# Kernel optimization log

Measured on AMD Instinct MI355X. Metric: run time of the kernel, lower is better.

The kernel has to match this reference:

```python
import jax, jax.numpy as jnp
import numpy as np
from jax import lax

TOP_NUMBER = 5
MOMENTUM = 0.1
EPS = 1e-12  # F.normalize eps


def _normalize(x):
    # F.normalize(x, dim=1): x / max(||x||_2, eps)
    n = jnp.sqrt(jnp.sum(x * x, axis=1, keepdims=True))
    return x / jnp.maximum(n, EPS)


def _cos_distance(a, b):
    # 0.5 * (1 - cos_sim); a:[B,D], b:[N,D] -> [B,N]
    a = _normalize(a)
    b = _normalize(b)
    return 0.5 * (1.0 - jnp.matmul(a, b.T))


def setup_inputs() -> dict:
    key = jax.random.key(0)
    ks = jax.random.split(key, 6)
    B, D, C, N = 64, 256, 345, 200000
    return {
        "target_feature": jax.random.normal(ks[0], (B, D), dtype=jnp.float32),
        "fc1": jax.random.normal(ks[1], (B, C), dtype=jnp.float32),
        "fc2": jax.random.normal(ks[2], (B, C), dtype=jnp.float32),
        "index_target": jnp.arange(B, dtype=jnp.int64 if jax.config.jax_enable_x64 else jnp.int32),
        "target_featurememory": jax.random.normal(ks[3], (N, D), dtype=jnp.float32),
        "target_softmaxFc1memory": jax.random.uniform(ks[4], (N, C), dtype=jnp.float32),
        "target_softmaxFc2memory": jax.random.uniform(ks[5], (N, C), dtype=jnp.float32),
    }


def reference(target_feature, fc1, fc2, index_target,
              target_featurememory, target_softmaxFc1memory, target_softmaxFc2memory):
    k = TOP_NUMBER
    m = MOMENTUM

    # predict(): softmax first
    fc1 = jax.nn.softmax(fc1, axis=1)
    fc2 = jax.nn.softmax(fc2, axis=1)

    # update(): momentum scatter-update of the memory banks (uses .data, i.e. detached)
    feat_mem = target_featurememory.at[index_target].set(
        (1.0 - m) * target_featurememory[index_target] + m * target_feature)
    fc1_mem = target_softmaxFc1memory.at[index_target].set(
        (1.0 - m) * target_softmaxFc1memory[index_target] + m * fc1)
    fc2_mem = target_softmaxFc2memory.at[index_target].set(
        (1.0 - m) * target_softmaxFc2memory[index_target] + m * fc2)

    # feature_smiliarity: nearest (smallest cos-distance) features, drop self (first)
    d_feat = _cos_distance(target_feature, feat_mem)          # [B, N]
    _, idx = lax.top_k(-d_feat, k + 1)                         # smallest distances
    idx = idx[:, 1:].reshape(-1)                               # [B*k]
    fc1_gather = fc1_mem[idx]                                  # [B*k, C]
    fc2_gather = fc2_mem[idx]
    loss_softmax = jnp.mean(jnp.abs(fc1_gather - fc2_gather))  # Discrepancy (L1)

    # softmax_smiliarity: topk of size k, then drop first -> k-1 neighbors
    d1 = _cos_distance(fc1, fc1_mem)                           # [B, N]
    _, i1 = lax.top_k(-d1, k)
    i1 = i1[:, 1:].reshape(-1)                                 # [B*(k-1)]
    feat1 = feat_mem[i1]                                       # [B*(k-1), D]

    d2 = _cos_distance(fc2, fc2_mem)
    _, i2 = lax.top_k(-d2, k)
    i2 = i2[:, 1:].reshape(-1)
    feat2 = feat_mem[i2]

    # FeatureDistance: 0.5 * (1 - <norm(a), norm(b)>) per row, then mean
    fd = 0.5 * (1.0 - jnp.sum(_normalize(feat1) * _normalize(feat2), axis=1))
    loss_feature = jnp.mean(fd)

    return (loss_softmax, loss_feature)
```

## Files before the change

### kernel.cpp

```cpp
#include <hip/hip_runtime.h>
#include <hip/hip_bf16.h>
#include <float.h>
#include <math.h>

#define NQ    64
#define DF    256
#define CC    345
#define KSF   8
#define KSC   11
#define NBM   768
#define FRESH (1 << 30)
#define EPSN  1e-12f

typedef __attribute__((ext_vector_type(8))) short short8;
typedef __attribute__((ext_vector_type(4))) float f32x4;

__device__ __forceinline__ void gld16(const void* g, void* l) {
  __builtin_amdgcn_global_load_lds(
      static_cast<const uint32_t*>(g), static_cast<uint32_t*>(l), 16, 0, 0);
}
__device__ __forceinline__ void gld4(const void* g, void* l) {
  __builtin_amdgcn_global_load_lds(
      static_cast<const uint32_t*>(g), static_cast<uint32_t*>(l), 4, 0, 0);
}

__device__ __forceinline__ float blockReduceSum(float v, float* sbuf) {
  __syncthreads();
  #pragma unroll
  for (int o = 32; o > 0; o >>= 1) v += __shfl_down(v, o);
  int w = threadIdx.x >> 6;
  if ((threadIdx.x & 63) == 0) sbuf[w] = v;
  __syncthreads();
  if (threadIdx.x == 0) {
    float s = 0.f;
    int nw = blockDim.x >> 6;
    for (int i = 0; i < nw; ++i) s += sbuf[i];
    sbuf[0] = s;
  }
  __syncthreads();
  return sbuf[0];
}

__device__ __forceinline__ float blockReduceMax(float v, float* sbuf) {
  __syncthreads();
  #pragma unroll
  for (int o = 32; o > 0; o >>= 1) v = fmaxf(v, __shfl_down(v, o));
  int w = threadIdx.x >> 6;
  if ((threadIdx.x & 63) == 0) sbuf[w] = v;
  __syncthreads();
  if (threadIdx.x == 0) {
    float s = -FLT_MAX;
    int nw = blockDim.x >> 6;
    for (int i = 0; i < nw; ++i) s = fmaxf(s, sbuf[i]);
    sbuf[0] = s;
  }
  __syncthreads();
  return sbuf[0];
}

template<int T>
__device__ __forceinline__ void topk_insert(float v, int id, float (&lv)[T], int (&li)[T]) {
  if (!((v > lv[T-1]) || (v == lv[T-1] && id < li[T-1]))) return;
  #pragma unroll
  for (int p = T-1; p > 0; --p) {
    bool up = (v > lv[p-1]) || (v == lv[p-1] && id < li[p-1]);
    if (up) { lv[p] = lv[p-1]; li[p] = li[p-1]; }
    else    { lv[p] = v; li[p] = id; return; }
  }
  lv[0] = v; li[0] = id;
}

template<int T>
__device__ __forceinline__ void merge4(const float* sv, const int* si, int t,
                                       float* dv, int* di) {
  float fv[T]; int fi[T];
  #pragma unroll
  for (int i = 0; i < T; ++i) { fv[i] = -FLT_MAX; fi[i] = 0x7fffffff; }
  for (int s = 0; s < 4; ++s)
    #pragma unroll
    for (int i = 0; i < T; ++i)
      topk_insert<T>(sv[(t*4+s)*T+i], si[(t*4+s)*T+i], fv, fi);
  #pragma unroll
  for (int i = 0; i < T; ++i) { dv[t*T+i] = fv[i]; di[t*T+i] = fi[i]; }
}

__global__ void fill_rowmap(int* rowmap, int n) {
  int i = blockIdx.x * blockDim.x + threadIdx.x;
  if (i < n) rowmap[i] = -1;
}

__global__ __launch_bounds__(384) void prep_kernel(
    const float* __restrict__ tf, const float* __restrict__ fc1,
    const float* __restrict__ fc2, const int* __restrict__ idx,
    const float* __restrict__ featm, const float* __restrict__ fc1m,
    const float* __restrict__ fc2m,
    short* __restrict__ Qp_feat, short* __restrict__ Qp_fc1, short* __restrict__ Qp_fc2,
    float* __restrict__ featU, float* __restrict__ fc1U, float* __restrict__ fc2U,
    int* __restrict__ rowmap)
{
  __shared__ float sbuf[8];
  const int b = blockIdx.x, t = threadIdx.x;
  const int trow = idx[b];
  const int qt = b >> 4, qr = b & 15;

  {
    float x = (t < DF) ? tf[b*DF + t] : 0.f;
    float ss = blockReduceSum(x*x, sbuf);
    float inv = 1.f / fmaxf(sqrtf(ss), EPSN);
    if (t < DF) {
      featU[b*DF + t] = 0.9f * featm[(size_t)trow*DF + t] + 0.1f * x;
      int ks = t >> 5, lg = (t >> 3) & 3, j = t & 7;
      int lane = qr + lg*16;
      union { __hip_bfloat16 h; short s; } cv;
      cv.h = __float2bfloat16(x * inv);
      Qp_feat[((qt*KSF + ks)*64 + lane)*8 + j] = cv.s;
    }
  }
  {
    float y = (t < CC) ? fc1[b*CC + t] : -FLT_MAX;
    float mx = blockReduceMax(y, sbuf);
    float e = (t < CC) ? expf(y - mx) : 0.f;
    float se = blockReduceSum(e, sbuf);
    float s = e / se;
    float s2 = blockReduceSum(s*s, sbuf);
    float inv2 = 1.f / fmaxf(sqrtf(s2), EPSN);
    if (t < CC) fc1U[b*CC + t] = 0.9f * fc1m[(size_t)trow*CC + t] + 0.1f * s;
    if (t < KSC*32) {
      int ks = t >> 5, lg = (t >> 3) & 3, j = t & 7;
      int lane = qr + lg*16;
      union { __hip_bfloat16 h; short s; } cv;
      cv.h = __float2bfloat16((t < CC) ? s * inv2 : 0.f);
      Qp_fc1[((qt*KSC + ks)*64 + lane)*8 + j] = cv.s;
    }
  }
  {
    float y = (t < CC) ? fc2[b*CC + t] : -FLT_MAX;
    float mx = blockReduceMax(y, sbuf);
    float e = (t < CC) ? expf(y - mx) : 0.f;
    float se = blockReduceSum(e, sbuf);
    float s = e / se;
    float s2 = blockReduceSum(s*s, sbuf);
    float inv2 = 1.f / fmaxf(sqrtf(s2), EPSN);
    if (t < CC) fc2U[b*CC + t] = 0.9f * fc2m[(size_t)trow*CC + t] + 0.1f * s;
    if (t < KSC*32) {
      int ks = t >> 5, lg = (t >> 3) & 3, j = t & 7;
      int lane = qr + lg*16;
      union { __hip_bfloat16 h; short s; } cv;
      cv.h = __float2bfloat16((t < CC) ? s * inv2 : 0.f);
      Qp_fc2[((qt*KSC + ks)*64 + lane)*8 + j] = cv.s;
    }
  }
  if (t == 0) rowmap[trow] = b;
}

template<int D, int KS, int T>
__global__ __launch_bounds__(256, 3) void dist_topk5(
    const float* __restrict__ bank, const float* __restrict__ ubank,
    const int* __restrict__ uids, const short8* __restrict__ Qp,
    float* __restrict__ cand_v, int* __restrict__ cand_i,
    int nmain, int ntq, int ntr)
{
  constexpr bool FEAT = (D == 256);
  constexpr int GROW = D * 4;
  constexpr int SROW = FEAT ? 1024 : 1392;
  constexpr int BUFB = 16 * SROW;

  __shared__ __align__(16) char smem[2*BUFB + 128 + 2*64*17*4];
  char*  k344 = smem + 2*BUFB;
  float* sims = (float*)(smem + 2*BUFB + 128);
  float* mv   = (float*)smem;
  int*   mi   = (int*)(smem + 256*T*4);

  const int t = threadIdx.x, l = t & 63, w = t >> 6;
  const int lc = l & 15, lg = l >> 4;
  const bool corr = ((int)blockIdx.x >= nmain);
  const float* srcb = corr ? ubank : bank;

  int tile0, nt;
  if (corr) { tile0 = blockIdx.x - nmain; nt = 1; }
  else {
    int b = blockIdx.x;
    tile0 = b*ntq + (b < ntr ? b : ntr);
    nt = ntq + (b < ntr ? 1 : 0);
  }

  short8 afr[KS];
  #pragma unroll
  for (int ks = 0; ks < KS; ++ks) afr[ks] = Qp[(w*KS + ks)*64 + l];

  auto STAGE = [&](int tile, int pn) {
    const char* tb = (const char*)srcb + (size_t)tile * (size_t)(16*GROW);
    char* bb = smem + pn*BUFB;
    #pragma unroll
    for (int r2 = 0; r2 < 4; ++r2) {
      int row = w*4 + r2;
      if (FEAT) {
        gld16(tb + row*1024 + ((l ^ (row & 7)) * 16), bb + row*1024);
      } else {
        gld16(tb + row*1380 + l*16, bb + row*1392);
        if (l < 22) gld16(tb + row*1380 + 1024 + l*16, bb + row*1392 + 1024);
      }
    }
    if (!FEAT && w == 0 && l < 16)
      gld4(tb + l*1380 + 1376, k344 + pn*64);
  };

  STAGE(tile0, 0);
  __syncthreads();

  float lv[T]; int li[T];
  #pragma unroll
  for (int i = 0; i < T; ++i) { lv[i] = -FLT_MAX; li[i] = 0x7fffffff; }

  for (int it = 0; it < nt; ++it) {
    const int pn = it & 1;
    if (it + 1 < nt) STAGE(tile0 + it + 1, pn ^ 1);

    const char* bb = smem + pn*BUFB;
    f32x4 acc = (f32x4){0.f, 0.f, 0.f, 0.f};
    float sq = 0.f;

    #pragma unroll
    for (int ks = 0; ks < KS; ++ks) {
      float v[8];
      if (!FEAT && ks == KS-1 && lg == 3) {
        v[0] = *(const float*)(k344 + pn*64 + lc*4);
        #pragma unroll
        for (int j = 1; j < 8; ++j) v[j] = 0.f;
      } else if (FEAT) {
        int g0 = ks*8 + lg*2;
        float4 a = *(const float4*)(bb + lc*1024 + ((g0 ^ (lc & 7)) * 16));
        float4 c = *(const float4*)(bb + lc*1024 + (((g0 + 1) ^ (lc & 7)) * 16));
        v[0]=a.x; v[1]=a.y; v[2]=a.z; v[3]=a.w;
        v[4]=c.x; v[5]=c.y; v[6]=c.z; v[7]=c.w;
      } else {
        const char* p = bb + lc*1392 + ks*128 + lg*32;
        float4 a = *(const float4*)p;
        float4 c = *(const float4*)(p + 16);
        v[0]=a.x; v[1]=a.y; v[2]=a.z; v[3]=a.w;
        v[4]=c.x; v[5]=c.y; v[6]=c.z; v[7]=c.w;
      }
      #pragma unroll
      for (int j = 0; j < 8; ++j) sq += v[j]*v[j];
      union { short8 s8; __hip_bfloat162 h2[4]; } fb;
      #pragma unroll
      for (int j = 0; j < 4; ++j)
        fb.h2[j] = __float22bfloat162_rn(make_float2(v[2*j], v[2*j+1]));
      acc = __builtin_amdgcn_mfma_f32_16x16x32_bf16(afr[ks], fb.s8, acc, 0, 0, 0);
    }

    float s = sq;
    s += __shfl_xor(s, 16);
    s += __shfl_xor(s, 32);
    float ri = 1.f / fmaxf(sqrtf(s), EPSN);

    float* sp = sims + pn*64*17;
    #pragma unroll
    for (int rg = 0; rg < 4; ++rg)
      sp[(w*16 + lg*4 + rg)*17 + lc] = acc[rg] * ri;
    __syncthreads();

    {
      int q = t & 63, sub = t >> 6;
      const float* s2 = sims + pn*64*17 + q*17 + sub*4;
      #pragma unroll
      for (int j = 0; j < 4; ++j) {
        int r = sub*4 + j;
        int id = corr ? (uids[tile0*16 + r] | FRESH) : ((tile0 + it)*16 + r);
        topk_insert<T>(s2[j], id, lv, li);
      }
    }
  }
  __syncthreads();

  #pragma unroll
  for (int i = 0; i < T; ++i) { mv[t*T + i] = lv[i]; mi[t*T + i] = li[i]; }
  __syncthreads();
  if (t < 64) {
    float fv[T]; int fi[T];
    #pragma unroll
    for (int i = 0; i < T; ++i) { fv[i] = -FLT_MAX; fi[i] = 0x7fffffff; }
    for (int s = 0; s < 4; ++s) {
      int srcidx = t + 64*s;
      #pragma unroll
      for (int i = 0; i < T; ++i)
        topk_insert<T>(mv[srcidx*T + i], mi[srcidx*T + i], fv, fi);
    }
    size_t base = ((size_t)blockIdx.x*64 + t)*T;
    #pragma unroll
    for (int i = 0; i < T; ++i) { cand_v[base + i] = fv[i]; cand_i[base + i] = fi[i]; }
  }
}

template<int T>
__global__ __launch_bounds__(256) void merge_stage1(
    const float* __restrict__ cv, const int* __restrict__ ci,
    const int* __restrict__ rowmap, int nslots,
    float* __restrict__ midv, int* __restrict__ midi)
{
  __shared__ float sv[256*T]; __shared__ int si[256*T];
  __shared__ float sv2[64*T]; __shared__ int si2[64*T];
  const int q = blockIdx.x >> 3, s = blockIdx.x & 7, t = threadIdx.x;
  const int len = (nslots + 7) >> 3;
  const int lo = s*len, hi = min(nslots, lo + len);
  float lv[T]; int li[T];
  #pragma unroll
  for (int i = 0; i < T; ++i) { lv[i] = -FLT_MAX; li[i] = 0x7fffffff; }
  for (int c = lo + t; c < hi; c += 256) {
    size_t base = ((size_t)c*64 + q)*T;
    #pragma unroll
    for (int i = 0; i < T; ++i) {
      int id = ci[base + i];
      if ((id & FRESH) || rowmap[id] < 0)
        topk_insert<T>(cv[base + i], id, lv, li);
    }
  }
  #pragma unroll
  for (int i = 0; i < T; ++i) { sv[t*T+i] = lv[i]; si[t*T+i] = li[i]; }
  __syncthreads();
  if (t < 64) merge4<T>(sv, si, t, sv2, si2);
  __syncthreads();
  if (t < 16) merge4<T>(sv2, si2, t, sv, si);
  __syncthreads();
  if (t < 4)  merge4<T>(sv, si, t, sv2, si2);
  __syncthreads();
  if (t == 0) {
    float fv[T]; int fi[T];
    #pragma unroll
    for (int i = 0; i < T; ++i) { fv[i] = -FLT_MAX; fi[i] = 0x7fffffff; }
    for (int c = 0; c < 4*T; ++c) topk_insert<T>(sv2[c], si2[c], fv, fi);
    #pragma unroll
    for (int i = 0; i < T; ++i) {
      midv[blockIdx.x*T + i] = fv[i];
      midi[blockIdx.x*T + i] = fi[i];
    }
  }
}

template<int T>
__global__ __launch_bounds__(64) void merge_stage2(
    const float* __restrict__ midv, const int* __restrict__ midi,
    int* __restrict__ topout)
{
  __shared__ float sv[8*T]; __shared__ int si[8*T];
  const int q = blockIdx.x, t = threadIdx.x;
  if (t < 8*T) { sv[t] = midv[q*8*T + t]; si[t] = midi[q*8*T + t]; }
  __syncthreads();
  if (t == 0) {
    float fv[T]; int fi[T];
    #pragma unroll
    for (int i = 0; i < T; ++i) { fv[i] = -FLT_MAX; fi[i] = 0x7fffffff; }
    for (int c = 0; c < 8*T; ++c) topk_insert<T>(sv[c], si[c], fv, fi);
    #pragma unroll
    for (int i = 0; i < T; ++i) topout[q*6 + i] = fi[i] & ~FRESH;
  }
}

__global__ __launch_bounds__(384) void loss_softmax_kernel(
    const int* __restrict__ topfeat, const int* __restrict__ rowmap,
    const float* __restrict__ fc1m, const float* __restrict__ fc1U,
    const float* __restrict__ fc2m, const float* __restrict__ fc2U,
    float* __restrict__ out)
{
  __shared__ float sbuf[8];
  int p = blockIdx.x;
  int q = p / 5, j = p % 5 + 1;
  int row = topfeat[q*6 + j];
  int u = rowmap[row];
  const float* r1 = (u >= 0) ? (fc1U + (size_t)u * CC) : (fc1m + (size_t)row * CC);
  const float* r2 = (u >= 0) ? (fc2U + (size_t)u * CC) : (fc2m + (size_t)row * CC);
  int t = threadIdx.x;
  float v = (t < CC) ? fabsf(r1[t] - r2[t]) : 0.f;
  float s = blockReduceSum(v, sbuf);
  if (t == 0) atomicAdd(out, s * (1.f / (320.f * 345.f)));
}

__global__ __launch_bounds__(256) void loss_feature_kernel(
    const int* __restrict__ topfc1, const int* __restrict__ topfc2,
    const int* __restrict__ rowmap, const float* __restrict__ featm,
    const float* __restrict__ featU, float* __restrict__ out)
{
  __shared__ float sbuf[8];
  int p = blockIdx.x;
  int q = p / 4, j = p % 4 + 1;
  int ra = topfc1[q*6 + j], rb = topfc2[q*6 + j];
  int ua = rowmap[ra], ub = rowmap[rb];
  const float* A  = (ua >= 0) ? (featU + (size_t)ua * DF) : (featm + (size_t)ra * DF);
  const float* Bp = (ub >= 0) ? (featU + (size_t)ub * DF) : (featm + (size_t)rb * DF);
  int t = threadIdx.x;
  float a = A[t], b = Bp[t];
  float saa = blockReduceSum(a*a, sbuf);
  float sbb = blockReduceSum(b*b, sbuf);
  float sab = blockReduceSum(a*b, sbuf);
  if (t == 0) {
    float fd = 0.5f * (1.f - sab / (fmaxf(sqrtf(saa), EPSN) * fmaxf(sqrtf(sbb), EPSN)));
    atomicAdd(out + 1, fd * (1.f / 256.f));
  }
}

extern "C" void kernel_launch(void* const* d_in, const int* in_sizes, int n_in,
                              void* d_out, int out_size, void* d_ws, size_t ws_size,
                              hipStream_t stream)
{
  const float* tf    = (const float*)d_in[0];
  const float* fc1   = (const float*)d_in[1];
  const float* fc2   = (const float*)d_in[2];
  const int*   idx   = (const int*)d_in[3];
  const float* featm = (const float*)d_in[4];
  const float* fc1m  = (const float*)d_in[5];
  const float* fc2m  = (const float*)d_in[6];
  float* out = (float*)d_out;

  const int N     = in_sizes[4] / DF;
  const int TILES = N / 16;
  const int NTQ   = TILES / NBM;
  const int NTR   = TILES - NTQ * NBM;
  const int NSLOT = NBM + 4;

  char* w = (char*)d_ws;
  auto alloc = [&](size_t bytes) {
    char* p = w;
    w += (bytes + 255) & ~(size_t)255;
    return (void*)p;
  };
  short* Qp_feat = (short*)alloc((size_t)4 * KSF * 64 * 8 * 2);
  short* Qp_fc1  = (short*)alloc((size_t)4 * KSC * 64 * 8 * 2);
  short* Qp_fc2  = (short*)alloc((size_t)4 * KSC * 64 * 8 * 2);
  float* featU   = (float*)alloc((size_t)NQ * DF * 4);
  float* fc1U    = (float*)alloc((size_t)NQ * CC * 4);
  float* fc2U    = (float*)alloc((size_t)NQ * CC * 4);
  int*   rowmap  = (int*)alloc((size_t)N * 4);
  int*   topfeat = (int*)alloc(NQ * 6 * 4);
  int*   topfc1  = (int*)alloc(NQ * 6 * 4);
  int*   topfc2  = (int*)alloc(NQ * 6 * 4);
  float* cand_v  = (float*)alloc((size_t)NSLOT * 64 * 6 * 4);
  int*   cand_i  = (int*)alloc((size_t)NSLOT * 64 * 6 * 4);
  float* midv    = (float*)alloc((size_t)NQ * 8 * 6 * 4);
  int*   midi    = (int*)alloc((size_t)NQ * 8 * 6 * 4);

  hipMemsetAsync(d_out, 0, 2 * sizeof(float), stream);
  fill_rowmap<<<(N + 255) / 256, 256, 0, stream>>>(rowmap, N);
  prep_kernel<<<NQ, 384, 0, stream>>>(tf, fc1, fc2, idx, featm, fc1m, fc2m,
      Qp_feat, Qp_fc1, Qp_fc2, featU, fc1U, fc2U, rowmap);

  dist_topk5<DF, KSF, 6><<<NSLOT, 256, 0, stream>>>(
      featm, featU, idx, (const short8*)Qp_feat, cand_v, cand_i, NBM, NTQ, NTR);
  merge_stage1<6><<<NQ*8, 256, 0, stream>>>(cand_v, cand_i, rowmap, NSLOT, midv, midi);
  merge_stage2<6><<<NQ, 64, 0, stream>>>(midv, midi, topfeat);

  dist_topk5<CC, KSC, 5><<<NSLOT, 256, 0, stream>>>(
      fc1m, fc1U, idx, (const short8*)Qp_fc1, cand_v, cand_i, NBM, NTQ, NTR);
  merge_stage1<5><<<NQ*8, 256, 0, stream>>>(cand_v, cand_i, rowmap, NSLOT, midv, midi);
  merge_stage2<5><<<NQ, 64, 0, stream>>>(midv, midi, topfc1);

  dist_topk5<CC, KSC, 5><<<NSLOT, 256, 0, stream>>>(
      fc2m, fc2U, idx, (const short8*)Qp_fc2, cand_v, cand_i, NBM, NTQ, NTR);
  merge_stage1<5><<<NQ*8, 256, 0, stream>>>(cand_v, cand_i, rowmap, NSLOT, midv, midi);
  merge_stage2<5><<<NQ, 64, 0, stream>>>(midv, midi, topfc2);

  loss_softmax_kernel<<<320, 384, 0, stream>>>(topfeat, rowmap, fc1m, fc1U, fc2m, fc2U, out);
  loss_feature_kernel<<<256, 256, 0, stream>>>(topfc1, topfc2, rowmap, featm, featU, out);
}
```

Baseline: 678.2 us.

## Prefetch two tiles ahead with explicit vmcnt waits and raw barriers

Restructures the double-buffered tile loop in the distance/top-k kernel. Two tiles are now staged up front, and each iteration waits on partial vmcnt counts so that the next tile's global-to-LDS loads stay in flight during compute. The next-next tile is issued into the freed buffer right after the sims barrier. It also replaces hipMemsetAsync with a tiny zeroing kernel. The hand-counted waitcnt values depend on exactly how many loads each wave issues, so a miscount could cause reads of stale LDS data.

After: 678.1 us. About the same (-0.0%).

```diff
diff --git a/kernel.cpp b/kernel.cpp
--- a/kernel.cpp
+++ b/kernel.cpp
@@ -22,6 +22,36 @@
 __device__ __forceinline__ void gld4(const void* g, void* l) {
   __builtin_amdgcn_global_load_lds(
       static_cast<const uint32_t*>(g), static_cast<uint32_t*>(l), 4, 0, 0);
+}
+
+__device__ __forceinline__ void wait_vm0() {
+  asm volatile("s_waitcnt vmcnt(0)" ::: "memory");
+  __builtin_amdgcn_sched_barrier(0);
+}
+__device__ __forceinline__ void wait_vm4() {
+  asm volatile("s_waitcnt vmcnt(4)" ::: "memory");
+  __builtin_amdgcn_sched_barrier(0);
+}
+__device__ __forceinline__ void wait_vm8() {
+  asm volatile("s_waitcnt vmcnt(8)" ::: "memory");
+  __builtin_amdgcn_sched_barrier(0);
+}
+__device__ __forceinline__ void wait_vm9() {
+  asm volatile("s_waitcnt vmcnt(9)" ::: "memory");
+  __builtin_amdgcn_sched_barrier(0);
+}
+__device__ __forceinline__ void wait_lgkm0() {
+  asm volatile("s_waitcnt lgkmcnt(0)" ::: "memory");
+  __builtin_amdgcn_sched_barrier(0);
+}
+__device__ __forceinline__ void raw_barrier() {
+  __builtin_amdgcn_sched_barrier(0);
+  __builtin_amdgcn_s_barrier();
+  __builtin_amdgcn_sched_barrier(0);
+}
+
+__global__ void zero_out(float* out) {
+  if (threadIdx.x < 2) out[threadIdx.x] = 0.f;
 }
 
 __device__ __forceinline__ float blockReduceSum(float v, float* sbuf) {
@@ -154,7 +184,7 @@
 }
 
 template<int D, int KS, int T>
-__global__ __launch_bounds__(256, 3) void dist_topk5(
+__global__ __launch_bounds__(256, 3) void dist_topk6(
     const float* __restrict__ bank, const float* __restrict__ ubank,
     const int* __restrict__ uids, const short8* __restrict__ Qp,
     float* __restrict__ cand_v, int* __restrict__ cand_i,
@@ -206,7 +236,7 @@
   };
 
   STAGE(tile0, 0);
-  __syncthreads();
+  if (nt > 1) STAGE(tile0 + 1, 1);
 
   float lv[T]; int li[T];
   #pragma unroll
@@ -214,7 +244,15 @@
 
   for (int it = 0; it < nt; ++it) {
     const int pn = it & 1;
-    if (it + 1 < nt) STAGE(tile0 + it + 1, pn ^ 1);
+
+    if (it + 1 < nt) {
+      if (FEAT) wait_vm4();
+      else if (w == 0) wait_vm9();
+      else wait_vm8();
+    } else {
+      wait_vm0();
+    }
+    raw_barrier();
 
     const char* bb = smem + pn*BUFB;
     f32x4 acc = (f32x4){0.f, 0.f, 0.f, 0.f};
@@ -258,7 +296,11 @@
     #pragma unroll
     for (int rg = 0; rg < 4; ++rg)
       sp[(w*16 + lg*4 + rg)*17 + lc] = acc[rg] * ri;
-    __syncthreads();
+
+    wait_lgkm0();
+    raw_barrier();
+
+    if (it + 2 < nt) STAGE(tile0 + it + 2, pn);
 
     {
       int q = t & 63, sub = t >> 6;
@@ -438,22 +480,22 @@
   float* midv    = (float*)alloc((size_t)NQ * 8 * 6 * 4);
   int*   midi    = (int*)alloc((size_t)NQ * 8 * 6 * 4);
 
-  hipMemsetAsync(d_out, 0, 2 * sizeof(float), stream);
+  zero_out<<<1, 64, 0, stream>>>(out);
   fill_rowmap<<<(N + 255) / 256, 256, 0, stream>>>(rowmap, N);
   prep_kernel<<<NQ, 384, 0, stream>>>(tf, fc1, fc2, idx, featm, fc1m, fc2m,
       Qp_feat, Qp_fc1, Qp_fc2, featU, fc1U, fc2U, rowmap);
 
-  dist_topk5<DF, KSF, 6><<<NSLOT, 256, 0, stream>>>(
+  dist_topk6<DF, KSF, 6><<<NSLOT, 256, 0, stream>>>(
       featm, featU, idx, (const short8*)Qp_feat, cand_v, cand_i, NBM, NTQ, NTR);
   merge_stage1<6><<<NQ*8, 256, 0, stream>>>(cand_v, cand_i, rowmap, NSLOT, midv, midi);
   merge_stage2<6><<<NQ, 64, 0, stream>>>(midv, midi, topfeat);
 
-  dist_topk5<CC, KSC, 5><<<NSLOT, 256, 0, stream>>>(
+  dist_topk6<CC, KSC, 5><<<NSLOT, 256, 0, stream>>>(
       fc1m, fc1U, idx, (const short8*)Qp_fc1, cand_v, cand_i, NBM, NTQ, NTR);
   merge_stage1<5><<<NQ*8, 256, 0, stream>>>(cand_v, cand_i, rowmap, NSLOT, midv, midi);
   merge_stage2<5><<<NQ, 64, 0, stream>>>(midv, midi, topfc1);
 
-  dist_topk5<CC, KSC, 5><<<NSLOT, 256, 0, stream>>>(
+  dist_topk6<CC, KSC, 5><<<NSLOT, 256, 0, stream>>>(
       fc2m, fc2U, idx, (const short8*)Qp_fc2, cand_v, cand_i, NBM, NTQ, NTR);
   merge_stage1<5><<<NQ*8, 256, 0, stream>>>(cand_v, cand_i, rowmap, NSLOT, midv, midi);
   merge_stage2<5><<<NQ, 64, 0, stream>>>(midv, midi, topfc2);
```

## Restructure distance-topk to per-wave tiles with direct global loads

Applied to the files above, without the earlier changes.

Replaces the block-cooperative LDS-staged, double-buffered distance kernel with a per-wave design. Each wave loads its 16-row tile straight from global memory, computes all 64 query columns with four MFMA accumulators, and keeps its own top-k with no block-level syncs or in-block merge. Each wave writes its own candidate slot, which greatly increases the number of candidates merge_stage1 has to process. The aim is to remove __syncthreads and LDS staging overhead and raise occupancy, at the cost of uncoalesced per-lane row loads, query fragments re-read from global memory for every tile, and a heavier merge step.

Measured after the change: 1.129 ms. 1.67x slower.

```diff
diff --git a/kernel.cpp b/kernel.cpp
--- a/kernel.cpp
+++ b/kernel.cpp
@@ -8,20 +8,18 @@
 #define CC    345
 #define KSF   8
 #define KSC   11
-#define NBM   768
+#define BLK   512
+#define NBLK  768
+#define NWAVES (NBLK * (BLK/64))
 #define FRESH (1 << 30)
 #define EPSN  1e-12f
 
 typedef __attribute__((ext_vector_type(8))) short short8;
 typedef __attribute__((ext_vector_type(4))) float f32x4;
-
-__device__ __forceinline__ void gld16(const void* g, void* l) {
-  __builtin_amdgcn_global_load_lds(
-      static_cast<const uint32_t*>(g), static_cast<uint32_t*>(l), 16, 0, 0);
-}
-__device__ __forceinline__ void gld4(const void* g, void* l) {
-  __builtin_amdgcn_global_load_lds(
-      static_cast<const uint32_t*>(g), static_cast<uint32_t*>(l), 4, 0, 0);
+typedef __attribute__((ext_vector_type(4), aligned(4))) float f32x4u;
+
+__global__ void zero_out(float* out) {
+  if (threadIdx.x < 2) out[threadIdx.x] = 0.f;
 }
 
 __device__ __forceinline__ float blockReduceSum(float v, float* sbuf) {
@@ -154,91 +152,45 @@
 }
 
 template<int D, int KS, int T>
-__global__ __launch_bounds__(256, 3) void dist_topk5(
+__global__ __launch_bounds__(BLK, 4) void dist_topk7(
     const float* __restrict__ bank, const float* __restrict__ ubank,
     const int* __restrict__ uids, const short8* __restrict__ Qp,
-    float* __restrict__ cand_v, int* __restrict__ cand_i,
-    int nmain, int ntq, int ntr)
-{
-  constexpr bool FEAT = (D == 256);
-  constexpr int GROW = D * 4;
-  constexpr int SROW = FEAT ? 1024 : 1392;
-  constexpr int BUFB = 16 * SROW;
-
-  __shared__ __align__(16) char smem[2*BUFB + 128 + 2*64*17*4];
-  char*  k344 = smem + 2*BUFB;
-  float* sims = (float*)(smem + 2*BUFB + 128);
-  float* mv   = (float*)smem;
-  int*   mi   = (int*)(smem + 256*T*4);
-
-  const int t = threadIdx.x, l = t & 63, w = t >> 6;
+    float* __restrict__ cand_v, int* __restrict__ cand_i, int ntm)
+{
+  __shared__ __align__(16) float scr[BLK/64][16*68];
+  const int t = threadIdx.x, l = t & 63;
   const int lc = l & 15, lg = l >> 4;
-  const bool corr = ((int)blockIdx.x >= nmain);
-  const float* srcb = corr ? ubank : bank;
-
-  int tile0, nt;
-  if (corr) { tile0 = blockIdx.x - nmain; nt = 1; }
-  else {
-    int b = blockIdx.x;
-    tile0 = b*ntq + (b < ntr ? b : ntr);
-    nt = ntq + (b < ntr ? 1 : 0);
-  }
-
-  short8 afr[KS];
-  #pragma unroll
-  for (int ks = 0; ks < KS; ++ks) afr[ks] = Qp[(w*KS + ks)*64 + l];
-
-  auto STAGE = [&](int tile, int pn) {
-    const char* tb = (const char*)srcb + (size_t)tile * (size_t)(16*GROW);
-    char* bb = smem + pn*BUFB;
-    #pragma unroll
-    for (int r2 = 0; r2 < 4; ++r2) {
-      int row = w*4 + r2;
-      if (FEAT) {
-        gld16(tb + row*1024 + ((l ^ (row & 7)) * 16), bb + row*1024);
-      } else {
-        gld16(tb + row*1380 + l*16, bb + row*1392);
-        if (l < 22) gld16(tb + row*1380 + 1024 + l*16, bb + row*1392 + 1024);
-      }
-    }
-    if (!FEAT && w == 0 && l < 16)
-      gld4(tb + l*1380 + 1376, k344 + pn*64);
-  };
-
-  STAGE(tile0, 0);
-  __syncthreads();
+  const int wloc = t >> 6;
+  const int wid = blockIdx.x * (BLK/64) + wloc;
+  const int TT = ntm + 4;
+  float* myscr = scr[wloc];
 
   float lv[T]; int li[T];
   #pragma unroll
   for (int i = 0; i < T; ++i) { lv[i] = -FLT_MAX; li[i] = 0x7fffffff; }
 
-  for (int it = 0; it < nt; ++it) {
-    const int pn = it & 1;
-    if (it + 1 < nt) STAGE(tile0 + it + 1, pn ^ 1);
-
-    const char* bb = smem + pn*BUFB;
-    f32x4 acc = (f32x4){0.f, 0.f, 0.f, 0.f};
+  for (int tile = wid; tile < TT; tile += NWAVES) {
+    const bool corr = (tile >= ntm);
+    const float* rp = corr
+        ? (ubank + ((size_t)(tile - ntm) * 16 + lc) * D)
+        : (bank  + ((size_t)tile * 16 + lc) * D);
+
+    f32x4 a0 = (f32x4){0.f,0.f,0.f,0.f};
+    f32x4 a1 = a0, a2 = a0, a3 = a0;
     float sq = 0.f;
 
     #pragma unroll
     for (int ks = 0; ks < KS; ++ks) {
       float v[8];
-      if (!FEAT && ks == KS-1 && lg == 3) {
-        v[0] = *(const float*)(k344 + pn*64 + lc*4);
+      if (D % 32 != 0 && ks == KS - 1 && lg == 3) {
+        v[0] = rp[D - 1];
         #pragma unroll
         for (int j = 1; j < 8; ++j) v[j] = 0.f;
-      } else if (FEAT) {
-        int g0 = ks*8 + lg*2;
-        float4 a = *(const float4*)(bb + lc*1024 + ((g0 ^ (lc & 7)) * 16));
-        float4 c = *(const float4*)(bb + lc*1024 + (((g0 + 1) ^ (lc & 7)) * 16));
-        v[0]=a.x; v[1]=a.y; v[2]=a.z; v[3]=a.w;
-        v[4]=c.x; v[5]=c.y; v[6]=c.z; v[7]=c.w;
       } else {
-        const char* p = bb + lc*1392 + ks*128 + lg*32;
-        float4 a = *(const float4*)p;
-        float4 c = *(const float4*)(p + 16);
-        v[0]=a.x; v[1]=a.y; v[2]=a.z; v[3]=a.w;
-        v[4]=c.x; v[5]=c.y; v[6]=c.z; v[7]=c.w;
+        const f32x4u* p = (const f32x4u*)(rp + ks*32 + lg*8);
+        f32x4u x = p[0], y = p[1];
+        v[0]=x[0]; v[1]=x[1]; v[2]=x[2]; v[3]=x[3];
+        v[4]=y[0]; v[5]=y[1]; v[6]=y[2]; v[7]=y[3];
       }
       #pragma unroll
       for (int j = 0; j < 8; ++j) sq += v[j]*v[j];
@@ -246,7 +198,10 @@
       #pragma unroll
       for (int j = 0; j < 4; ++j)
         fb.h2[j] = __float22bfloat162_rn(make_float2(v[2*j], v[2*j+1]));
-      acc = __builtin_amdgcn_mfma_f32_16x16x32_bf16(afr[ks], fb.s8, acc, 0, 0, 0);
+      a0 = __builtin_amdgcn_mfma_f32_16x16x32_bf16(Qp[(0*KS+ks)*64 + l], fb.s8, a0, 0,0,0);
+      a1 = __builtin_amdgcn_mfma_f32_16x16x32_bf16(Qp[(1*KS+ks)*64 + l], fb.s8, a1, 0,0,0);
+      a2 = __builtin_amdgcn_mfma_f32_16x16x32_bf16(Qp[(2*KS+ks)*64 + l], fb.s8, a2, 0,0,0);
+      a3 = __builtin_amdgcn_mfma_f32_16x16x32_bf16(Qp[(3*KS+ks)*64 + l], fb.s8, a3, 0,0,0);
     }
 
     float s = sq;
@@ -254,42 +209,31 @@
     s += __shfl_xor(s, 32);
     float ri = 1.f / fmaxf(sqrtf(s), EPSN);
 
-    float* sp = sims + pn*64*17;
-    #pragma unroll
-    for (int rg = 0; rg < 4; ++rg)
-      sp[(w*16 + lg*4 + rg)*17 + lc] = acc[rg] * ri;
-    __syncthreads();
-
-    {
-      int q = t & 63, sub = t >> 6;
-      const float* s2 = sims + pn*64*17 + q*17 + sub*4;
+    *(f32x4*)(myscr + lc*68 +  0 + lg*4) = a0 * ri;
+    *(f32x4*)(myscr + lc*68 + 16 + lg*4) = a1 * ri;
+    *(f32x4*)(myscr + lc*68 + 32 + lg*4) = a2 * ri;
+    *(f32x4*)(myscr + lc*68 + 48 + lg*4) = a3 * ri;
+
+    if (corr) {
+      const int ub = (tile - ntm) * 16;
       #pragma unroll
-      for (int j = 0; j < 4; ++j) {
-        int r = sub*4 + j;
-        int id = corr ? (uids[tile0*16 + r] | FRESH) : ((tile0 + it)*16 + r);
-        topk_insert<T>(s2[j], id, lv, li);
+      for (int j = 0; j < 16; ++j) {
+        float vv = myscr[j*68 + l];
+        topk_insert<T>(vv, uids[ub + j] | FRESH, lv, li);
       }
-    }
-  }
-  __syncthreads();
-
-  #pragma unroll
-  for (int i = 0; i < T; ++i) { mv[t*T + i] = lv[i]; mi[t*T + i] = li[i]; }
-  __syncthreads();
-  if (t < 64) {
-    float fv[T]; int fi[T];
-    #pragma unroll
-    for (int i = 0; i < T; ++i) { fv[i] = -FLT_MAX; fi[i] = 0x7fffffff; }
-    for (int s = 0; s < 4; ++s) {
-      int srcidx = t + 64*s;
+    } else {
+      const int gb = tile * 16;
       #pragma unroll
-      for (int i = 0; i < T; ++i)
-        topk_insert<T>(mv[srcidx*T + i], mi[srcidx*T + i], fv, fi);
-    }
-    size_t base = ((size_t)blockIdx.x*64 + t)*T;
-    #pragma unroll
-    for (int i = 0; i < T; ++i) { cand_v[base + i] = fv[i]; cand_i[base + i] = fi[i]; }
-  }
+      for (int j = 0; j < 16; ++j) {
+        float vv = myscr[j*68 + l];
+        topk_insert<T>(vv, gb + j, lv, li);
+      }
+    }
+  }
+
+  size_t base = ((size_t)wid * 64 + l) * T;
+  #pragma unroll
+  for (int i = 0; i < T; ++i) { cand_v[base + i] = lv[i]; cand_i[base + i] = li[i]; }
 }
 
 template<int T>
@@ -411,11 +355,8 @@
   const float* fc2m  = (const float*)d_in[6];
   float* out = (float*)d_out;
 
-  const int N     = in_sizes[4] / DF;
-  const int TILES = N / 16;
-  const int NTQ   = TILES / NBM;
-  const int NTR   = TILES - NTQ * NBM;
-  const int NSLOT = NBM + 4;
+  const int N   = in_sizes[4] / DF;
+  const int NTM = N / 16;
 
   char* w = (char*)d_ws;
   auto alloc = [&](size_t bytes) {
@@ -433,29 +374,29 @@
   int*   topfeat = (int*)alloc(NQ * 6 * 4);
   int*   topfc1  = (int*)alloc(NQ * 6 * 4);
   int*   topfc2  = (int*)alloc(NQ * 6 * 4);
-  float* cand_v  = (float*)alloc((size_t)NSLOT * 64 * 6 * 4);
-  int*   cand_i  = (int*)alloc((size_t)NSLOT * 64 * 6 * 4);
+  float* cand_v  = (float*)alloc((size_t)NWAVES * 64 * 6 * 4);
+  int*   cand_i  = (int*)alloc((size_t)NWAVES * 64 * 6 * 4);
   float* midv    = (float*)alloc((size_t)NQ * 8 * 6 * 4);
   int*   midi    = (int*)alloc((size_t)NQ * 8 * 6 * 4);
 
-  hipMemsetAsync(d_out, 0, 2 * sizeof(float), stream);
+  zero_out<<<1, 64, 0, stream>>>(out);
   fill_rowmap<<<(N + 255) / 256, 256, 0, stream>>>(rowmap, N);
   prep_kernel<<<NQ, 384, 0, stream>>>(tf, fc1, fc2, idx, featm, fc1m, fc2m,
       Qp_feat, Qp_fc1, Qp_fc2, featU, fc1U, fc2U, rowmap);
 
-  dist_topk5<DF, KSF, 6><<<NSLOT, 256, 0, stream>>>(
-      featm, featU, idx, (const short8*)Qp_feat, cand_v, cand_i, NBM, NTQ, NTR);
-  merge_stage1<6><<<NQ*8, 256, 0, stream>>>(cand_v, cand_i, rowmap, NSLOT, midv, midi);
+  dist_topk7<DF, KSF, 6><<<NBLK, BLK, 0, stream>>>(
+      featm, featU, idx, (const short8*)Qp_feat, cand_v, cand_i, NTM);
+  merge_stage1<6><<<NQ*8, 256, 0, stream>>>(cand_v, cand_i, rowmap, NWAVES, midv, midi);
   merge_stage2<6><<<NQ, 64, 0, stream>>>(midv, midi, topfeat);
 
-  dist_topk5<CC, KSC, 5><<<NSLOT, 256, 0, stream>>>(
-      fc1m, fc1U, idx, (const short8*)Qp_fc1, cand_v, cand_i, NBM, NTQ, NTR);
-  merge_stage1<5><<<NQ*8, 256, 0, stream>>>(cand_v, cand_i, rowmap, NSLOT, midv, midi);
+  dist_topk7<CC, KSC, 5><<<NBLK, BLK, 0, stream>>>(
+      fc1m, fc1U, idx, (const short8*)Qp_fc1, cand_v, cand_i, NTM);
+  merge_stage1<5><<<NQ*8, 256, 0, stream>>>(cand_v, cand_i, rowmap, NWAVES, midv, midi);
   merge_stage2<5><<<NQ, 64, 0, stream>>>(midv, midi, topfc1);
 
-  dist_topk5<CC, KSC, 5><<<NSLOT, 256, 0, stream>>>(
-      fc2m, fc2U, idx, (const short8*)Qp_fc2, cand_v, cand_i, NBM, NTQ, NTR);
-  merge_stage1<5><<<NQ*8, 256, 0, stream>>>(cand_v, cand_i, rowmap, NSLOT, midv, midi);
+  dist_topk7<CC, KSC, 5><<<NBLK, BLK, 0, stream>>>(
+      fc2m, fc2U, idx, (const short8*)Qp_fc2, cand_v, cand_i, NTM);
+  merge_stage1<5><<<NQ*8, 256, 0, stream>>>(cand_v, cand_i, rowmap, NWAVES, midv, midi);
   merge_stage2<5><<<NQ, 64, 0, stream>>>(midv, midi, topfc2);
 
   loss_softmax_kernel<<<320, 384, 0, stream>>>(topfeat, rowmap, fc1m, fc1U, fc2m, fc2U, out);
```
